# Kernel tuning notes

Measured on AMD Instinct MI355X. Metric: run time of the kernel, lower is better.

Reference implementation:

```python
import jax, jax.numpy as jnp
import numpy as np

H = 8          # num heads
D = 16         # head dim
HID = 128      # hidden_dim = H * D
NM, ND, NA = 100000, 20000, 50000
E = 300000     # edges per relation
NUM_CLASSES = 8


def setup_inputs() -> dict:
    key = jax.random.key(0)
    ks = jax.random.split(key, 24)
    s = 0.05
    eye = jnp.eye(D, dtype=jnp.float32)
    inp = {
        'x_movie': jax.random.normal(ks[0], (NM, 256), jnp.float32),
        'x_director': jax.random.normal(ks[1], (ND, 128), jnp.float32),
        'x_actor': jax.random.normal(ks[2], (NA, 128), jnp.float32),
        # edge lists per relation: (director->movie, actor->movie, movie->director, movie->actor)
        'src_dm': jax.random.randint(ks[3], (E,), 0, ND),
        'dst_dm': jax.random.randint(ks[4], (E,), 0, NM),
        'src_am': jax.random.randint(ks[5], (E,), 0, NA),
        'dst_am': jax.random.randint(ks[6], (E,), 0, NM),
        'src_md': jax.random.randint(ks[7], (E,), 0, NM),
        'dst_md': jax.random.randint(ks[8], (E,), 0, ND),
        'src_ma': jax.random.randint(ks[9], (E,), 0, NM),
        'dst_ma': jax.random.randint(ks[10], (E,), 0, NA),
        # per-type pre-encoder (use_pre_encoder=True)
        'Wpre_m': jax.random.normal(ks[11], (256, HID), jnp.float32) * s,
        'Wpre_d': jax.random.normal(ks[12], (128, HID), jnp.float32) * s,
        'Wpre_a': jax.random.normal(ks[13], (128, HID), jnp.float32) * s,
        'bpre': jnp.zeros((3, HID), jnp.float32),
        # per-type K/Q/V projections, stacked over the 3 node types
        'Wk': jax.random.normal(ks[14], (3, HID, HID), jnp.float32) * s,
        'bk': jnp.zeros((3, HID), jnp.float32),
        'Wq': jax.random.normal(ks[15], (3, HID, HID), jnp.float32) * s,
        'bq': jnp.zeros((3, HID), jnp.float32),
        'Wv': jax.random.normal(ks[16], (3, HID, HID), jnp.float32) * s,
        'bv': jnp.zeros((3, HID), jnp.float32),
        # per-relation attention / message matrices and priors (4 relations)
        'a_rel': eye + jax.random.normal(ks[17], (4, H, D, D), jnp.float32) * s,
        'm_rel': eye + jax.random.normal(ks[18], (4, H, D, D), jnp.float32) * s,
        'p_rel': jnp.ones((4, H), jnp.float32),
        # per-type skip gate and output projection
        'skip': jnp.ones((3,), jnp.float32),
        'Wa': jax.random.normal(ks[19], (3, HID, HID), jnp.float32) * s,
        'ba': jnp.zeros((3, HID), jnp.float32),
        # final classification head on target node type ('movie')
        'Wlin': jax.random.normal(ks[20], (HID, NUM_CLASSES), jnp.float32) * s,
        'blin': jnp.zeros((NUM_CLASSES,), jnp.float32),
    }
    return inp


def _seg_softmax_agg(alpha, msg, dst, n):
    # softmax over incoming edges of each destination node, then weighted sum of msgs
    m = jax.ops.segment_max(alpha, dst, num_segments=n)      # [n, H]
    m = jnp.where(jnp.isfinite(m), m, 0.0)
    a = jnp.exp(alpha - m[dst])                              # [E, H]
    denom = jax.ops.segment_sum(a, dst, num_segments=n)      # [n, H]
    num = jax.ops.segment_sum(a[:, :, None] * msg, dst, num_segments=n)  # [n, H, D]
    return num / jnp.maximum(denom, 1e-16)[:, :, None]


def reference(x_movie, x_director, x_actor,
              src_dm, dst_dm, src_am, dst_am, src_md, dst_md, src_ma, dst_ma,
              Wpre_m, Wpre_d, Wpre_a, bpre, Wk, bk, Wq, bq, Wv, bv,
              a_rel, m_rel, p_rel, skip, Wa, ba, Wlin, blin):
    # type order: 0=movie, 1=director, 2=actor
    xs = [x_movie @ Wpre_m + bpre[0],
          x_director @ Wpre_d + bpre[1],
          x_actor @ Wpre_a + bpre[2]]
    k = [(x @ Wk[t] + bk[t]).reshape(-1, H, D) for t, x in enumerate(xs)]
    q = [(x @ Wq[t] + bq[t]).reshape(-1, H, D) for t, x in enumerate(xs)]
    v = [(x @ Wv[t] + bv[t]).reshape(-1, H, D) for t, x in enumerate(xs)]

    # (src_type, dst_type, src_idx, dst_idx) per relation
    rels = [(1, 0, src_dm, dst_dm), (2, 0, src_am, dst_am),
            (0, 1, src_md, dst_md), (0, 2, src_ma, dst_ma)]
    scale = 1.0 / np.sqrt(D).astype(np.float32)
    buckets = {0: [], 1: [], 2: []}
    for r, (st, dt, src, dst) in enumerate(rels):
        ke = jnp.einsum('ehd,hdf->ehf', k[st][src], a_rel[r])          # [E,H,D]
        al = jnp.einsum('ehf,ehf->eh', q[dt][dst], ke) * p_rel[r] * scale
        me = jnp.einsum('ehd,hdf->ehf', v[st][src], m_rel[r])          # [E,H,D]
        buckets[dt].append((al, me, dst))

    n = [x.shape[0] for x in xs]
    outs = []
    for t in range(3):
        al = jnp.concatenate([b[0] for b in buckets[t]], axis=0)
        me = jnp.concatenate([b[1] for b in buckets[t]], axis=0)
        dst = jnp.concatenate([b[2] for b in buckets[t]], axis=0)
        agg = _seg_softmax_agg(al, me, dst, n[t]).reshape(n[t], HID)
        h = jax.nn.gelu(agg, approximate=False) @ Wa[t] + ba[t]
        g = jax.nn.sigmoid(skip[t])
        outs.append(g * h + (1.0 - g) * xs[t])

    return outs[0] @ Wlin + blin
```

## Files before the change

kernel.cpp:

```cpp
#include <hip/hip_runtime.h>
#include <hip/hip_bf16.h>
#include <math.h>

#define NM 100000
#define ND 20000
#define NA 50000
#define EDG 300000
#define CAP 32
#define NBLK_M 1563
#define NBLK_D 313
#define NBLK_A 782

typedef __attribute__((ext_vector_type(8))) short shortx8;
typedef __attribute__((ext_vector_type(4))) float floatx4;
typedef __attribute__((ext_vector_type(4))) int intx4;

__device__ __forceinline__ float bf2f(unsigned int u) {
    return __uint_as_float(u << 16);
}
__device__ __forceinline__ unsigned short f2bf(float f) {
    unsigned int x = __float_as_uint(f);
    unsigned int r = x + 0x7fffu + ((x >> 16) & 1u);
    return (unsigned short)(r >> 16);
}
__device__ __forceinline__ unsigned short f2bf_fast(float f) {
    return (unsigned short)((__float_as_uint(f) + 0x8000u) >> 16);
}
__device__ __forceinline__ unsigned int pkbf2(float a, float b) {
    return __builtin_amdgcn_perm(__float_as_uint(b) + 0x8000u,
                                 __float_as_uint(a) + 0x8000u,
                                 0x07060302u);
}
__device__ __forceinline__ float gelu_exact(float x) {
    return 0.5f * x * (1.0f + erff(x * 0.70710678118654752f));
}

static const size_t OFF_BT_Q      = 0;
static const size_t OFF_BT_KAMV_D = 73728;
static const size_t OFF_BT_KAMV_A = 139264;
static const size_t OFF_WKA_D     = 204800;
static const size_t OFF_WVM_D     = 270336;
static const size_t OFF_WKA_A     = 335872;
static const size_t OFF_WVM_A     = 401408;
static const size_t OFF_BQ        = 466944;
static const size_t OFF_B_KAMV_D  = 467520;
static const size_t OFF_B_KAMV_A  = 468544;
static const size_t OFF_BKA_D     = 469568;
static const size_t OFF_BVM_D     = 470080;
static const size_t OFF_BKA_A     = 470592;
static const size_t OFF_BVM_A     = 471104;
static const size_t OFF_WALS      = 471616;
static const size_t OFF_BFIN      = 475712;
static const size_t OFF_Q0        = 524288;
static const size_t OFF_SKIPB     = 26124288;
static const size_t OFF_WQT       = 26124288;
static const size_t OFF_KAMV_D    = 29324288;
static const size_t OFF_KAMV_A    = 39564288;
static const size_t OFF_COUNTS    = 65164288;
static const size_t OFF_SLOTS     = 65564288;
#define KAMV_A_DELTA 10240000

__global__ __launch_bounds__(256) void precompA(
    const float* __restrict__ Wk, const float* __restrict__ bk,
    const float* __restrict__ Wv, const float* __restrict__ bv,
    const float* __restrict__ Wa, const float* __restrict__ ba,
    const float* __restrict__ Wlin, const float* __restrict__ blin,
    const float* __restrict__ a_rel, const float* __restrict__ m_rel,
    const float* __restrict__ p_rel, const float* __restrict__ skip,
    const float* __restrict__ bpre, const float* __restrict__ Wq,
    char* __restrict__ ws)
{
    int tid = blockIdx.x * 256 + threadIdx.x;
    if (tid < 65536) {
        int mat = tid >> 14, rem = tid & 16383;
        int e = rem >> 7, hf = rem & 127, h = hf >> 4, f = hf & 15;
        const float* Wsrc; const float* R; float sc; float* dst;
        if (mat == 0)      { Wsrc = Wk + 16384; R = a_rel;        sc = p_rel[h]     * 0.25f; dst = (float*)(ws + OFF_WKA_D); }
        else if (mat == 1) { Wsrc = Wv + 16384; R = m_rel;        sc = 1.0f;                 dst = (float*)(ws + OFF_WVM_D); }
        else if (mat == 2) { Wsrc = Wk + 32768; R = a_rel + 2048; sc = p_rel[8 + h] * 0.25f; dst = (float*)(ws + OFF_WKA_A); }
        else               { Wsrc = Wv + 32768; R = m_rel + 2048; sc = 1.0f;                 dst = (float*)(ws + OFF_WVM_A); }
        float s = 0.0f;
        for (int d = 0; d < 16; d++)
            s += Wsrc[e * 128 + h * 16 + d] * R[h * 256 + d * 16 + f];
        dst[hf * 128 + e] = s * sc;
    } else if (tid < 66048) {
        int idx = tid - 65536;
        int mat = idx >> 7, hf = idx & 127, h = hf >> 4, f = hf & 15;
        const float* bsrc; const float* R; float sc; float* dst;
        if (mat == 0)      { bsrc = bk + 128; R = a_rel;        sc = p_rel[h]     * 0.25f; dst = (float*)(ws + OFF_BKA_D); }
        else if (mat == 1) { bsrc = bv + 128; R = m_rel;        sc = 1.0f;                 dst = (float*)(ws + OFF_BVM_D); }
        else if (mat == 2) { bsrc = bk + 256; R = a_rel + 2048; sc = p_rel[8 + h] * 0.25f; dst = (float*)(ws + OFF_BKA_A); }
        else               { bsrc = bv + 256; R = m_rel + 2048; sc = 1.0f;                 dst = (float*)(ws + OFF_BVM_A); }
        float s = 0.0f;
        for (int d = 0; d < 16; d++)
            s += bsrc[h * 16 + d] * R[h * 256 + d * 16 + f];
        dst[hf] = s * sc;
    } else if (tid < 67072) {
        int idx = tid - 66048;
        int j = idx >> 3, c = idx & 7;
        float g = 1.0f / (1.0f + __expf(-skip[0]));
        float s = 0.0f;
        for (int o = 0; o < 128; o++)
            s += Wa[j * 128 + o] * Wlin[o * 8 + c];
        ((float*)(ws + OFF_WALS))[j * 8 + c] = g * s;
    } else if (tid < 67080) {
        int c = tid - 67072;
        float g = 1.0f / (1.0f + __expf(-skip[0]));
        float s1 = 0.0f, s2 = 0.0f;
        for (int o = 0; o < 128; o++) {
            s1 += ba[o]   * Wlin[o * 8 + c];
            s2 += bpre[o] * Wlin[o * 8 + c];
        }
        ((float*)(ws + OFF_BFIN))[c] = g * s1 + (1.0f - g) * s2 + blin[c];
    } else if (tid < 83464) {
        int i = tid - 67080;
        int n = i >> 7, e = i & 127;
        ((float*)(ws + OFF_WQT))[n * 128 + e] = Wq[e * 128 + n];
    } else if (tid < 83464 + NM) {
        ((int*)(ws + OFF_COUNTS))[tid - 83464] = 0;
    }
}

__device__ __forceinline__ float dot128(const float* __restrict__ a,
                                        const float* __restrict__ b) {
    const floatx4* x = (const floatx4*)a;
    const floatx4* y = (const floatx4*)b;
    float s = 0.0f;
    #pragma unroll
    for (int i = 0; i < 32; i++) {
        floatx4 u = x[i], v = y[i];
        s += u[0] * v[0] + u[1] * v[1] + u[2] * v[2] + u[3] * v[3];
    }
    return s;
}

__global__ __launch_bounds__(256) void prep_scat(
    const int* __restrict__ src_dm, const int* __restrict__ dst_dm,
    const int* __restrict__ src_am, const int* __restrict__ dst_am,
    const float* __restrict__ Wpre_m, const float* __restrict__ Wpre_d,
    const float* __restrict__ Wpre_a, const float* __restrict__ bpre,
    const float* __restrict__ bq, const float* __restrict__ Wlin,
    const float* __restrict__ skip,
    char* __restrict__ ws)
{
    if (blockIdx.x < 2344) {
        int t = blockIdx.x * 256 + threadIdx.x;
        if (t >= 2 * EDG) return;
        int src, dst, delta;
        if (t < EDG) { src = src_dm[t];       dst = dst_dm[t];       delta = 0; }
        else         { src = src_am[t - EDG]; dst = dst_am[t - EDG]; delta = KAMV_A_DELTA; }
        int* counts = (int*)(ws + OFF_COUNTS);
        int* slots  = (int*)(ws + OFF_SLOTS);
        int pos = atomicAdd(&counts[dst], 1);
        if (pos < CAP) slots[(size_t)dst * CAP + pos] = src * 512 + delta;
        return;
    }
    int tid = (blockIdx.x - 2344) * 256 + threadIdx.x;
    const float* WKA_D = (const float*)(ws + OFF_WKA_D);
    const float* WVM_D = (const float*)(ws + OFF_WVM_D);
    const float* WKA_A = (const float*)(ws + OFF_WKA_A);
    const float* WVM_A = (const float*)(ws + OFF_WVM_A);
    const float* WqT   = (const float*)(ws + OFF_WQT);

    if (tid < 36864) {
        int n = tid >> 8, c = tid & 255;
        float s = 0.0f;
        if (n < 128) {
            s = dot128(Wpre_m + c * 128, WqT + n * 128);
        } else if (n < 136) {
            int cc = n - 128;
            float g = 1.0f / (1.0f + __expf(-skip[0]));
            for (int e = 0; e < 128; e++)
                s += Wpre_m[c * 128 + e] * Wlin[e * 8 + cc];
            s *= (1.0f - g);
        }
        ((unsigned short*)(ws + OFF_BT_Q))[(c >> 7) * 18432 + n * 128 + (c & 127)] = f2bf(s);
    } else if (tid < 69632) {
        int idx = tid - 36864;
        int nrow = idx >> 7, c = idx & 127;
        const float* WfT = (nrow < 128) ? WKA_D : WVM_D;
        int nc = nrow & 127;
        float s = dot128(Wpre_d + c * 128, WfT + nc * 128);
        ((unsigned short*)(ws + OFF_BT_KAMV_D))[nrow * 128 + c] = f2bf(s);
    } else if (tid < 102400) {
        int idx = tid - 69632;
        int nrow = idx >> 7, c = idx & 127;
        const float* WfT = (nrow < 128) ? WKA_A : WVM_A;
        int nc = nrow & 127;
        float s = dot128(Wpre_a + c * 128, WfT + nc * 128);
        ((unsigned short*)(ws + OFF_BT_KAMV_A))[nrow * 128 + c] = f2bf(s);
    } else if (tid < 102544) {
        int n = tid - 102400;
        float s = 0.0f;
        if (n < 128) s = dot128(bpre, WqT + n * 128) + bq[n];
        ((float*)(ws + OFF_BQ))[n] = s;
    } else if (tid < 102800) {
        int nrow = tid - 102544;
        const float* WfT = (nrow < 128) ? WKA_D : WVM_D;
        const float* bf_ = (nrow < 128) ? (const float*)(ws + OFF_BKA_D) : (const float*)(ws + OFF_BVM_D);
        int nc = nrow & 127;
        ((float*)(ws + OFF_B_KAMV_D))[nrow] = dot128(bpre + 128, WfT + nc * 128) + bf_[nc];
    } else if (tid < 103056) {
        int nrow = tid - 102800;
        const float* WfT = (nrow < 128) ? WKA_A : WVM_A;
        const float* bf_ = (nrow < 128) ? (const float*)(ws + OFF_BKA_A) : (const float*)(ws + OFF_BVM_A);
        int nc = nrow & 127;
        ((float*)(ws + OFF_B_KAMV_A))[nrow] = dot128(bpre + 256, WfT + nc * 128) + bf_[nc];
    }
}

#define MFMA16(a, b, c) __builtin_amdgcn_mfma_f32_16x16x32_bf16(a, b, c, 0, 0, 0)

__global__ __launch_bounds__(256, 2) void gemm_all(
    const float* __restrict__ xm, const float* __restrict__ xd,
    const float* __restrict__ xa,
    const unsigned short* __restrict__ btq,
    const unsigned short* __restrict__ btd,
    const unsigned short* __restrict__ bta,
    const float* __restrict__ bq,
    const float* __restrict__ bbd, const float* __restrict__ bba,
    unsigned short* __restrict__ q0, float* __restrict__ skipb,
    unsigned short* __restrict__ outd, unsigned short* __restrict__ outa)
{
    __shared__ unsigned short a_lds[64 * 136];
    __shared__ unsigned short b_lds[144 * 136];
    int tid = threadIdx.x;
    int w = tid >> 6, lane = tid & 63;
    int quad = lane >> 4, low = lane & 15;
    int bx = blockIdx.x;

    if (bx < NBLK_M) {
        int row0 = bx * 64;
        intx4 bv[9];
        #pragma unroll
        for (int it = 0; it < 9; it++) {
            int idx = it * 256 + tid, n = idx >> 4, ch = idx & 15;
            bv[it] = *(const intx4*)&btq[(size_t)n * 128 + ch * 8];
        }
        floatx4 av[8];
        #pragma unroll
        for (int it = 0; it < 8; it++) {
            int f = it * 256 + tid, r = f >> 5, c4 = f & 31;
            int rg = row0 + r; if (rg >= NM) rg = NM - 1;
            av[it] = *(const floatx4*)(xm + (size_t)rg * 256 + c4 * 4);
        }
        #pragma unroll
        for (int it = 0; it < 9; it++) {
            int idx = it * 256 + tid, n = idx >> 4, ch = idx & 15;
            *(intx4*)&b_lds[n * 136 + ch * 8] = bv[it];
        }
        #pragma unroll
        for (int it = 0; it < 8; it++) {
            int f = it * 256 + tid, r = f >> 5, c4 = f & 31;
            unsigned long long d =
                ((unsigned long long)pkbf2(av[it][2], av[it][3]) << 32) |
                pkbf2(av[it][0], av[it][1]);
            *(unsigned long long*)&a_lds[r * 136 + c4 * 4] = d;
        }
        __syncthreads();

        intx4 bv1[9];
        #pragma unroll
        for (int it = 0; it < 9; it++) {
            int idx = it * 256 + tid, n = idx >> 4, ch = idx & 15;
            bv1[it] = *(const intx4*)&btq[18432 + (size_t)n * 128 + ch * 8];
        }
        floatx4 av1[8];
        #pragma unroll
        for (int it = 0; it < 8; it++) {
            int f = it * 256 + tid, r = f >> 5, c4 = f & 31;
            int rg = row0 + r; if (rg >= NM) rg = NM - 1;
            av1[it] = *(const floatx4*)(xm + (size_t)rg * 256 + 128 + c4 * 4);
        }

        floatx4 acc[9] = {};
        #pragma unroll
        for (int ks = 0; ks < 4; ks++) {
            int ko = ks * 32 + quad * 8;
            shortx8 a0 = *(const shortx8*)&a_lds[(w * 16 + low) * 136 + ko];
            #pragma unroll
            for (int nt = 0; nt < 9; nt++) {
                shortx8 b = *(const shortx8*)&b_lds[(nt * 16 + low) * 136 + ko];
                acc[nt] = MFMA16(a0, b, acc[nt]);
            }
        }
        __syncthreads();
        #pragma unroll
        for (int it = 0; it < 9; it++) {
            int idx = it * 256 + tid, n = idx >> 4, ch = idx & 15;
            *(intx4*)&b_lds[n * 136 + ch * 8] = bv1[it];
        }
        #pragma unroll
        for (int it = 0; it < 8; it++) {
            int f = it * 256 + tid, r = f >> 5, c4 = f & 31;
            unsigned long long d =
                ((unsigned long long)pkbf2(av1[it][2], av1[it][3]) << 32) |
                pkbf2(av1[it][0], av1[it][1]);
            *(unsigned long long*)&a_lds[r * 136 + c4 * 4] = d;
        }
        __syncthreads();
        #pragma unroll
        for (int ks = 0; ks < 4; ks++) {
            int ko = ks * 32 + quad * 8;
            shortx8 a0 = *(const shortx8*)&a_lds[(w * 16 + low) * 136 + ko];
            #pragma unroll
            for (int nt = 0; nt < 9; nt++) {
                shortx8 b = *(const shortx8*)&b_lds[(nt * 16 + low) * 136 + ko];
                acc[nt] = MFMA16(a0, b, acc[nt]);
            }
        }

        int rb = row0 + w * 16;
        #pragma unroll
        for (int nt = 0; nt < 9; nt++) {
            #pragma unroll
            for (int r = 0; r < 4; r++) {
                int row = rb + quad * 4 + r;
                if (row >= NM) continue;
                int col = nt * 16 + low;
                float v = acc[nt][r] + bq[col];
                if (nt == 8) {
                    if (low < 8) skipb[(size_t)row * 8 + low] = v;
                } else {
                    q0[(size_t)row * 128 + col] = f2bf_fast(v);
                }
            }
        }
    } else {
        int rem = bx - NBLK_M;
        const float* A; const unsigned short* BT; const float* bias;
        unsigned short* outb; int M, kbx;
        if (rem < NBLK_D) { A = xd; BT = btd; bias = bbd; outb = outd; M = ND; kbx = rem; }
        else              { A = xa; BT = bta; bias = bba; outb = outa; M = NA; kbx = rem - NBLK_D; }
        int row0 = kbx * 64;

        intx4 bv[8];
        #pragma unroll
        for (int it = 0; it < 8; it++) {
            int idx = it * 256 + tid, n = idx >> 4, ch = idx & 15;
            bv[it] = *(const intx4*)&BT[(size_t)n * 128 + ch * 8];
        }
        floatx4 av[8];
        #pragma unroll
        for (int it = 0; it < 8; it++) {
            int f = it * 256 + tid, r = f >> 5, c4 = f & 31;
            int rg = row0 + r; if (rg >= M) rg = M - 1;
            av[it] = *(const floatx4*)(A + (size_t)rg * 128 + c4 * 4);
        }
        #pragma unroll
        for (int it = 0; it < 8; it++) {
            int idx = it * 256 + tid, n = idx >> 4, ch = idx & 15;
            *(intx4*)&b_lds[n * 136 + ch * 8] = bv[it];
        }
        #pragma unroll
        for (int it = 0; it < 8; it++) {
            int f = it * 256 + tid, r = f >> 5, c4 = f & 31;
            unsigned long long d =
                ((unsigned long long)pkbf2(av[it][2], av[it][3]) << 32) |
                pkbf2(av[it][0], av[it][1]);
            *(unsigned long long*)&a_lds[r * 136 + c4 * 4] = d;
        }
        __syncthreads();

        intx4 bv1[8];
        #pragma unroll
        for (int it = 0; it < 8; it++) {
            int idx = it * 256 + tid, n = idx >> 4, ch = idx & 15;
            bv1[it] = *(const intx4*)&BT[16384 + (size_t)n * 128 + ch * 8];
        }

        int rb = row0 + w * 16;
        {
            floatx4 acc[8] = {};
            #pragma unroll
            for (int ks = 0; ks < 4; ks++) {
                int ko = ks * 32 + quad * 8;
                shortx8 a0 = *(const shortx8*)&a_lds[(w * 16 + low) * 136 + ko];
                #pragma unroll
                for (int nt = 0; nt < 8; nt++) {
                    shortx8 b = *(const shortx8*)&b_lds[(nt * 16 + low) * 136 + ko];
                    acc[nt] = MFMA16(a0, b, acc[nt]);
                }
            }
            #pragma unroll
            for (int nt = 0; nt < 8; nt++) {
                #pragma unroll
                for (int r = 0; r < 4; r++) {
                    int row = rb + quad * 4 + r;
                    if (row >= M) continue;
                    int col = nt * 16 + low;
                    outb[(size_t)row * 256 + col] = f2bf_fast(acc[nt][r] + bias[col]);
                }
            }
        }
        __syncthreads();
        #pragma unroll
        for (int it = 0; it < 8; it++) {
            int idx = it * 256 + tid, n = idx >> 4, ch = idx & 15;
            *(intx4*)&b_lds[n * 136 + ch * 8] = bv1[it];
        }
        __syncthreads();
        {
            floatx4 acc[8] = {};
            #pragma unroll
            for (int ks = 0; ks < 4; ks++) {
                int ko = ks * 32 + quad * 8;
                shortx8 a0 = *(const shortx8*)&a_lds[(w * 16 + low) * 136 + ko];
                #pragma unroll
                for (int nt = 0; nt < 8; nt++) {
                    shortx8 b = *(const shortx8*)&b_lds[(nt * 16 + low) * 136 + ko];
                    acc[nt] = MFMA16(a0, b, acc[nt]);
                }
            }
            #pragma unroll
            for (int nt = 0; nt < 8; nt++) {
                #pragma unroll
                for (int r = 0; r < 4; r++) {
                    int row = rb + quad * 4 + r;
                    if (row >= M) continue;
                    int col = nt * 16 + low;
                    outb[(size_t)row * 256 + 128 + col] = f2bf_fast(acc[nt][r] + bias[128 + col]);
                }
            }
        }
    }
}

__global__ __launch_bounds__(256) void agg_kernel(
    const unsigned short* __restrict__ q0,
    const char* __restrict__ kamv0,
    const int* __restrict__ counts, const int* __restrict__ slots,
    const float* __restrict__ skipb,
    const float* __restrict__ WaLs, const float* __restrict__ bfin,
    float* __restrict__ out)
{
    __shared__ float wals[1032];
    for (int i = threadIdx.x; i < 1024; i += 256) {
        int c = i >> 7, rem = i & 127, j = rem >> 4, L = rem & 15;
        wals[i] = WaLs[(L * 8 + j) * 8 + c];
    }
    if (threadIdx.x < 8) wals[1024 + threadIdx.x] = bfin[threadIdx.x];
    __syncthreads();

    int lane = threadIdx.x & 63;
    int grp = lane >> 4;
    int L   = lane & 15;
    int n = blockIdx.x * 16 + (threadIdx.x >> 6) * 4 + grp;

    intx4 qv = *(const intx4*)(q0 + (size_t)n * 128 + L * 8);
    float qf[8];
    #pragma unroll
    for (int d = 0; d < 4; d++) {
        unsigned int u = (unsigned int)qv[d];
        qf[2 * d]     = __uint_as_float(u << 16);
        qf[2 * d + 1] = __uint_as_float(u & 0xffff0000u);
    }

    int cnt = counts[n];
    cnt = cnt < 0 ? 0 : (cnt > CAP ? CAP : cnt);
    int s0 = slots[(size_t)n * CAP + L];

    float acc[8] = {0, 0, 0, 0, 0, 0, 0, 0};
    float den = 0.0f;
    if (cnt > 0) {
        int off0 = __shfl(s0, lane & 48);
        const char* p = kamv0 + off0;
        intx4 ku = *(const intx4*)(p + L * 16);
        intx4 mu = *(const intx4*)(p + 256 + L * 16);
        for (int i = 0; i < cnt; i++) {
            int inext = (i + 1 < cnt) ? i + 1 : i;
            int offn = __shfl(s0, (lane & 48) + (inext & 15));
            if (__builtin_expect(inext >= 16, 0)) offn = slots[(size_t)n * CAP + inext];
            const char* pn = kamv0 + offn;
            intx4 kun = *(const intx4*)(pn + L * 16);
            intx4 mun = *(const intx4*)(pn + 256 + L * 16);

            float ph = 0.0f;
            #pragma unroll
            for (int d = 0; d < 4; d++) {
                unsigned int u = (unsigned int)ku[d];
                ph += qf[2 * d]     * __uint_as_float(u << 16);
                ph += qf[2 * d + 1] * __uint_as_float(u & 0xffff0000u);
            }
            float pf = ph + __shfl_xor(ph, 1);
            float wgt = __expf(fminf(pf, 60.0f));
            den += wgt;
            #pragma unroll
            for (int d = 0; d < 4; d++) {
                unsigned int u = (unsigned int)mu[d];
                acc[2 * d]     += wgt * __uint_as_float(u << 16);
                acc[2 * d + 1] += wgt * __uint_as_float(u & 0xffff0000u);
            }
            ku = kun; mu = mun;
        }
    }
    float inv = 1.0f / fmaxf(den, 1e-16f);

    float part[8] = {0, 0, 0, 0, 0, 0, 0, 0};
    #pragma unroll
    for (int j = 0; j < 8; j++) {
        float u = gelu_exact(acc[j] * inv);
        #pragma unroll
        for (int c = 0; c < 8; c++)
            part[c] += u * wals[c * 128 + j * 16 + L];
    }

    bool b0 = lane & 1, b1 = lane & 2, b2 = lane & 4;
    float t1[4], t2[2], t3;
    #pragma unroll
    for (int k = 0; k < 4; k++) {
        float send = b0 ? part[k] : part[4 + k];
        float got  = __shfl_xor(send, 1);
        t1[k] = (b0 ? part[4 + k] : part[k]) + got;
    }
    #pragma unroll
    for (int k = 0; k < 2; k++) {
        float send = b1 ? t1[k] : t1[2 + k];
        float got  = __shfl_xor(send, 2);
        t2[k] = (b1 ? t1[2 + k] : t1[k]) + got;
    }
    {
        float send = b2 ? t2[0] : t2[1];
        float got  = __shfl_xor(send, 4);
        t3 = (b2 ? t2[1] : t2[0]) + got;
    }
    t3 += __shfl_xor(t3, 8);
    if (L < 8) {
        int c = 4 * (L & 1) + 2 * ((L >> 1) & 1) + ((L >> 2) & 1);
        out[(size_t)n * 8 + c] = t3 + skipb[(size_t)n * 8 + c] + wals[1024 + c];
    }
}

extern "C" void kernel_launch(void* const* d_in, const int* in_sizes, int n_in,
                              void* d_out, int out_size, void* d_ws, size_t ws_size,
                              hipStream_t stream) {
    (void)in_sizes; (void)n_in; (void)out_size; (void)ws_size;
    const float* x_movie    = (const float*)d_in[0];
    const float* x_director = (const float*)d_in[1];
    const float* x_actor    = (const float*)d_in[2];
    const int* src_dm = (const int*)d_in[3];
    const int* dst_dm = (const int*)d_in[4];
    const int* src_am = (const int*)d_in[5];
    const int* dst_am = (const int*)d_in[6];
    const float* Wpre_m = (const float*)d_in[11];
    const float* Wpre_d = (const float*)d_in[12];
    const float* Wpre_a = (const float*)d_in[13];
    const float* bpre   = (const float*)d_in[14];
    const float* Wk     = (const float*)d_in[15];
    const float* bk     = (const float*)d_in[16];
    const float* Wq     = (const float*)d_in[17];
    const float* bq     = (const float*)d_in[18];
    const float* Wv     = (const float*)d_in[19];
    const float* bv     = (const float*)d_in[20];
    const float* a_rel  = (const float*)d_in[21];
    const float* m_rel  = (const float*)d_in[22];
    const float* p_rel  = (const float*)d_in[23];
    const float* skip   = (const float*)d_in[24];
    const float* Wa     = (const float*)d_in[25];
    const float* ba     = (const float*)d_in[26];
    const float* Wlin   = (const float*)d_in[27];
    const float* blin   = (const float*)d_in[28];

    char* ws = (char*)d_ws;
    float* out = (float*)d_out;

    precompA<<<(83464 + NM + 255) / 256, 256, 0, stream>>>(
        Wk, bk, Wv, bv, Wa, ba, Wlin, blin,
        a_rel, m_rel, p_rel, skip, bpre, Wq, ws);

    prep_scat<<<2344 + 403, 256, 0, stream>>>(
        src_dm, dst_dm, src_am, dst_am,
        Wpre_m, Wpre_d, Wpre_a, bpre, bq, Wlin, skip, ws);

    gemm_all<<<NBLK_M + NBLK_D + NBLK_A, 256, 0, stream>>>(
        x_movie, x_director, x_actor,
        (const unsigned short*)(ws + OFF_BT_Q),
        (const unsigned short*)(ws + OFF_BT_KAMV_D),
        (const unsigned short*)(ws + OFF_BT_KAMV_A),
        (const float*)(ws + OFF_BQ),
        (const float*)(ws + OFF_B_KAMV_D), (const float*)(ws + OFF_B_KAMV_A),
        (unsigned short*)(ws + OFF_Q0), (float*)(ws + OFF_SKIPB),
        (unsigned short*)(ws + OFF_KAMV_D), (unsigned short*)(ws + OFF_KAMV_A));

    agg_kernel<<<NM / 16, 256, 0, stream>>>(
        (const unsigned short*)(ws + OFF_Q0),
        (const char*)(ws + OFF_KAMV_D),
        (const int*)(ws + OFF_COUNTS), (const int*)(ws + OFF_SLOTS),
        (const float*)(ws + OFF_SKIPB),
        (const float*)(ws + OFF_WALS), (const float*)(ws + OFF_BFIN), out);
}
```

Before: 396.0 us.

## Make gemm_all persistent over 32-row tiles with register-prefetched next panel

Restructures the fused projection GEMM so each block loops over several 32-row tiles instead of one 64-row tile, and prefetches the next K-half or next tile's A and B data into registers while MFMAs run on the current LDS contents. Waves are split 2x2 over rows and column groups, the A tile is halved to raise occupancy to 3 blocks per CU, and the grid shrinks to about 760 blocks. The aim is to hide global load latency and cut the launch/tail cost of thousands of short blocks. In exchange, the B panel is reloaded from global memory for every tile and there are more barriers per output row, and the movie path drops the row bounds guard, relying on NM being divisible by 32.

```diff
diff --git a/kernel.cpp b/kernel.cpp
--- a/kernel.cpp
+++ b/kernel.cpp
@@ -7,9 +7,14 @@
 #define NA 50000
 #define EDG 300000
 #define CAP 32
-#define NBLK_M 1563
-#define NBLK_D 313
-#define NBLK_A 782
+
+#define NT_M   3125
+#define NT_D   625
+#define NT_K   2188
+#define T_M    7
+#define T_K    7
+#define BLK_M  447
+#define BLK_K  313
 
 typedef __attribute__((ext_vector_type(8))) short shortx8;
 typedef __attribute__((ext_vector_type(4))) float floatx4;
@@ -211,7 +216,7 @@
 
 #define MFMA16(a, b, c) __builtin_amdgcn_mfma_f32_16x16x32_bf16(a, b, c, 0, 0, 0)
 
-__global__ __launch_bounds__(256, 2) void gemm_all(
+__global__ __launch_bounds__(256, 3) void gemm_all(
     const float* __restrict__ xm, const float* __restrict__ xd,
     const float* __restrict__ xa,
     const unsigned short* __restrict__ btq,
@@ -222,204 +227,194 @@
     unsigned short* __restrict__ q0, float* __restrict__ skipb,
     unsigned short* __restrict__ outd, unsigned short* __restrict__ outa)
 {
-    __shared__ unsigned short a_lds[64 * 136];
+    __shared__ unsigned short a_lds[32 * 136];
     __shared__ unsigned short b_lds[144 * 136];
     int tid = threadIdx.x;
     int w = tid >> 6, lane = tid & 63;
     int quad = lane >> 4, low = lane & 15;
+    int g = w >> 1, s = w & 1;
     int bx = blockIdx.x;
 
-    if (bx < NBLK_M) {
-        int row0 = bx * 64;
+    if (bx < BLK_M) {
+        int tbase = bx * T_M;
+        floatx4 av[4];
         intx4 bv[9];
-        #pragma unroll
-        for (int it = 0; it < 9; it++) {
-            int idx = it * 256 + tid, n = idx >> 4, ch = idx & 15;
-            bv[it] = *(const intx4*)&btq[(size_t)n * 128 + ch * 8];
-        }
-        floatx4 av[8];
-        #pragma unroll
-        for (int it = 0; it < 8; it++) {
-            int f = it * 256 + tid, r = f >> 5, c4 = f & 31;
-            int rg = row0 + r; if (rg >= NM) rg = NM - 1;
-            av[it] = *(const floatx4*)(xm + (size_t)rg * 256 + c4 * 4);
-        }
-        #pragma unroll
-        for (int it = 0; it < 9; it++) {
-            int idx = it * 256 + tid, n = idx >> 4, ch = idx & 15;
-            *(intx4*)&b_lds[n * 136 + ch * 8] = bv[it];
-        }
-        #pragma unroll
-        for (int it = 0; it < 8; it++) {
-            int f = it * 256 + tid, r = f >> 5, c4 = f & 31;
-            unsigned long long d =
-                ((unsigned long long)pkbf2(av[it][2], av[it][3]) << 32) |
-                pkbf2(av[it][0], av[it][1]);
-            *(unsigned long long*)&a_lds[r * 136 + c4 * 4] = d;
-        }
-        __syncthreads();
-
-        intx4 bv1[9];
-        #pragma unroll
-        for (int it = 0; it < 9; it++) {
-            int idx = it * 256 + tid, n = idx >> 4, ch = idx & 15;
-            bv1[it] = *(const intx4*)&btq[18432 + (size_t)n * 128 + ch * 8];
-        }
-        floatx4 av1[8];
-        #pragma unroll
-        for (int it = 0; it < 8; it++) {
-            int f = it * 256 + tid, r = f >> 5, c4 = f & 31;
-            int rg = row0 + r; if (rg >= NM) rg = NM - 1;
-            av1[it] = *(const floatx4*)(xm + (size_t)rg * 256 + 128 + c4 * 4);
-        }
-
-        floatx4 acc[9] = {};
-        #pragma unroll
-        for (int ks = 0; ks < 4; ks++) {
-            int ko = ks * 32 + quad * 8;
-            shortx8 a0 = *(const shortx8*)&a_lds[(w * 16 + low) * 136 + ko];
-            #pragma unroll
-            for (int nt = 0; nt < 9; nt++) {
-                shortx8 b = *(const shortx8*)&b_lds[(nt * 16 + low) * 136 + ko];
-                acc[nt] = MFMA16(a0, b, acc[nt]);
-            }
-        }
-        __syncthreads();
-        #pragma unroll
-        for (int it = 0; it < 9; it++) {
-            int idx = it * 256 + tid, n = idx >> 4, ch = idx & 15;
-            *(intx4*)&b_lds[n * 136 + ch * 8] = bv1[it];
-        }
-        #pragma unroll
-        for (int it = 0; it < 8; it++) {
-            int f = it * 256 + tid, r = f >> 5, c4 = f & 31;
-            unsigned long long d =
-                ((unsigned long long)pkbf2(av1[it][2], av1[it][3]) << 32) |
-                pkbf2(av1[it][0], av1[it][1]);
-            *(unsigned long long*)&a_lds[r * 136 + c4 * 4] = d;
-        }
-        __syncthreads();
-        #pragma unroll
-        for (int ks = 0; ks < 4; ks++) {
-            int ko = ks * 32 + quad * 8;
-            shortx8 a0 = *(const shortx8*)&a_lds[(w * 16 + low) * 136 + ko];
-            #pragma unroll
-            for (int nt = 0; nt < 9; nt++) {
-                shortx8 b = *(const shortx8*)&b_lds[(nt * 16 + low) * 136 + ko];
-                acc[nt] = MFMA16(a0, b, acc[nt]);
-            }
-        }
-
-        int rb = row0 + w * 16;
-        #pragma unroll
-        for (int nt = 0; nt < 9; nt++) {
-            #pragma unroll
-            for (int r = 0; r < 4; r++) {
-                int row = rb + quad * 4 + r;
-                if (row >= NM) continue;
+        {
+            int row0 = (tbase < NT_M ? tbase : NT_M - 1) * 32;
+            #pragma unroll
+            for (int it = 0; it < 4; it++) {
+                int f = it * 256 + tid, r = f >> 5, c4 = f & 31;
+                av[it] = *(const floatx4*)(xm + (size_t)(row0 + r) * 256 + c4 * 4);
+            }
+            #pragma unroll
+            for (int it = 0; it < 9; it++) {
+                int idx = it * 256 + tid, n = idx >> 4, ch = idx & 15;
+                bv[it] = *(const intx4*)&btq[(size_t)n * 128 + ch * 8];
+            }
+        }
+        for (int t = 0; t < T_M; t++) {
+            int tcur = tbase + t;
+            if (tcur >= NT_M) break;
+            int row0 = tcur * 32;
+            floatx4 acc[5] = {};
+            #pragma unroll
+            for (int h = 0; h < 2; h++) {
+                __syncthreads();
+                #pragma unroll
+                for (int it = 0; it < 4; it++) {
+                    int f = it * 256 + tid, r = f >> 5, c4 = f & 31;
+                    unsigned long long d =
+                        ((unsigned long long)pkbf2(av[it][2], av[it][3]) << 32) |
+                        pkbf2(av[it][0], av[it][1]);
+                    *(unsigned long long*)&a_lds[r * 136 + c4 * 4] = d;
+                }
+                #pragma unroll
+                for (int it = 0; it < 9; it++) {
+                    int idx = it * 256 + tid, n = idx >> 4, ch = idx & 15;
+                    *(intx4*)&b_lds[n * 136 + ch * 8] = bv[it];
+                }
+                __syncthreads();
+                {
+                    int ntile = (h == 0) ? tcur : (tcur + 1 < NT_M ? tcur + 1 : NT_M - 1);
+                    int nh = 1 - h;
+                    int nrow0 = ntile * 32;
+                    #pragma unroll
+                    for (int it = 0; it < 4; it++) {
+                        int f = it * 256 + tid, r = f >> 5, c4 = f & 31;
+                        av[it] = *(const floatx4*)(xm + (size_t)(nrow0 + r) * 256 + nh * 128 + c4 * 4);
+                    }
+                    #pragma unroll
+                    for (int it = 0; it < 9; it++) {
+                        int idx = it * 256 + tid, n = idx >> 4, ch = idx & 15;
+                        bv[it] = *(const intx4*)&btq[(size_t)nh * 18432 + n * 128 + ch * 8];
+                    }
+                }
+                #pragma unroll
+                for (int ks = 0; ks < 4; ks++) {
+                    int ko = ks * 32 + quad * 8;
+                    shortx8 a0 = *(const shortx8*)&a_lds[(s * 16 + low) * 136 + ko];
+                    #pragma unroll
+                    for (int j = 0; j < 5; j++) {
+                        if (g == 1 && j == 4) continue;
+                        int nt = g * 5 + j;
+                        shortx8 b = *(const shortx8*)&b_lds[(nt * 16 + low) * 136 + ko];
+                        acc[j] = MFMA16(a0, b, acc[j]);
+                    }
+                }
+            }
+            #pragma unroll
+            for (int j = 0; j < 5; j++) {
+                if (g == 1 && j == 4) continue;
+                int nt = g * 5 + j;
                 int col = nt * 16 + low;
-                float v = acc[nt][r] + bq[col];
-                if (nt == 8) {
-                    if (low < 8) skipb[(size_t)row * 8 + low] = v;
+                #pragma unroll
+                for (int r = 0; r < 4; r++) {
+                    int row = row0 + s * 16 + quad * 4 + r;
+                    float v = acc[j][r] + bq[col];
+                    if (nt == 8) {
+                        if (low < 8) skipb[(size_t)row * 8 + low] = v;
+                    } else {
+                        q0[(size_t)row * 128 + col] = f2bf_fast(v);
+                    }
+                }
+            }
+        }
+    } else {
+        int kbase = (bx - BLK_M) * T_K;
+        floatx4 av[4];
+        intx4 bv[8];
+        {
+            int tt = kbase < NT_K ? kbase : NT_K - 1;
+            const float* A; int M, row0;
+            const unsigned short* BT;
+            if (tt < NT_D) { A = xd; M = ND; row0 = tt * 32; BT = btd; }
+            else           { A = xa; M = NA; row0 = (tt - NT_D) * 32; BT = bta; }
+            #pragma unroll
+            for (int it = 0; it < 4; it++) {
+                int f = it * 256 + tid, r = f >> 5, c4 = f & 31;
+                int rg = row0 + r; if (rg >= M) rg = M - 1;
+                av[it] = *(const floatx4*)(A + (size_t)rg * 128 + c4 * 4);
+            }
+            #pragma unroll
+            for (int it = 0; it < 8; it++) {
+                int idx = it * 256 + tid, n = idx >> 4, ch = idx & 15;
+                bv[it] = *(const intx4*)&BT[(size_t)n * 128 + ch * 8];
+            }
+        }
+        for (int t = 0; t < T_K; t++) {
+            int tcur = kbase + t;
+            if (tcur >= NT_K) break;
+            const float* A; int M, row0;
+            const unsigned short* BT; const float* bias;
+            unsigned short* outb;
+            if (tcur < NT_D) { A = xd; M = ND; row0 = tcur * 32; BT = btd; bias = bbd; outb = outd; }
+            else             { A = xa; M = NA; row0 = (tcur - NT_D) * 32; BT = bta; bias = bba; outb = outa; }
+
+            #pragma unroll
+            for (int pnl = 0; pnl < 2; pnl++) {
+                __syncthreads();
+                if (pnl == 0) {
+                    #pragma unroll
+                    for (int it = 0; it < 4; it++) {
+                        int f = it * 256 + tid, r = f >> 5, c4 = f & 31;
+                        unsigned long long d =
+                            ((unsigned long long)pkbf2(av[it][2], av[it][3]) << 32) |
+                            pkbf2(av[it][0], av[it][1]);
+                        *(unsigned long long*)&a_lds[r * 136 + c4 * 4] = d;
+                    }
+                }
+                #pragma unroll
+                for (int it = 0; it < 8; it++) {
+                    int idx = it * 256 + tid, n = idx >> 4, ch = idx & 15;
+                    *(intx4*)&b_lds[n * 136 + ch * 8] = bv[it];
+                }
+                __syncthreads();
+                if (pnl == 0) {
+                    #pragma unroll
+                    for (int it = 0; it < 8; it++) {
+                        int idx = it * 256 + tid, n = idx >> 4, ch = idx & 15;
+                        bv[it] = *(const intx4*)&BT[16384 + (size_t)n * 128 + ch * 8];
+                    }
                 } else {
-                    q0[(size_t)row * 128 + col] = f2bf_fast(v);
-                }
-            }
-        }
-    } else {
-        int rem = bx - NBLK_M;
-        const float* A; const unsigned short* BT; const float* bias;
-        unsigned short* outb; int M, kbx;
-        if (rem < NBLK_D) { A = xd; BT = btd; bias = bbd; outb = outd; M = ND; kbx = rem; }
-        else              { A = xa; BT = bta; bias = bba; outb = outa; M = NA; kbx = rem - NBLK_D; }
-        int row0 = kbx * 64;
-
-        intx4 bv[8];
-        #pragma unroll
-        for (int it = 0; it < 8; it++) {
-            int idx = it * 256 + tid, n = idx >> 4, ch = idx & 15;
-            bv[it] = *(const intx4*)&BT[(size_t)n * 128 + ch * 8];
-        }
-        floatx4 av[8];
-        #pragma unroll
-        for (int it = 0; it < 8; it++) {
-            int f = it * 256 + tid, r = f >> 5, c4 = f & 31;
-            int rg = row0 + r; if (rg >= M) rg = M - 1;
-            av[it] = *(const floatx4*)(A + (size_t)rg * 128 + c4 * 4);
-        }
-        #pragma unroll
-        for (int it = 0; it < 8; it++) {
-            int idx = it * 256 + tid, n = idx >> 4, ch = idx & 15;
-            *(intx4*)&b_lds[n * 136 + ch * 8] = bv[it];
-        }
-        #pragma unroll
-        for (int it = 0; it < 8; it++) {
-            int f = it * 256 + tid, r = f >> 5, c4 = f & 31;
-            unsigned long long d =
-                ((unsigned long long)pkbf2(av[it][2], av[it][3]) << 32) |
-                pkbf2(av[it][0], av[it][1]);
-            *(unsigned long long*)&a_lds[r * 136 + c4 * 4] = d;
-        }
-        __syncthreads();
-
-        intx4 bv1[8];
-        #pragma unroll
-        for (int it = 0; it < 8; it++) {
-            int idx = it * 256 + tid, n = idx >> 4, ch = idx & 15;
-            bv1[it] = *(const intx4*)&BT[16384 + (size_t)n * 128 + ch * 8];
-        }
-
-        int rb = row0 + w * 16;
-        {
-            floatx4 acc[8] = {};
-            #pragma unroll
-            for (int ks = 0; ks < 4; ks++) {
-                int ko = ks * 32 + quad * 8;
-                shortx8 a0 = *(const shortx8*)&a_lds[(w * 16 + low) * 136 + ko];
-                #pragma unroll
-                for (int nt = 0; nt < 8; nt++) {
-                    shortx8 b = *(const shortx8*)&b_lds[(nt * 16 + low) * 136 + ko];
-                    acc[nt] = MFMA16(a0, b, acc[nt]);
-                }
-            }
-            #pragma unroll
-            for (int nt = 0; nt < 8; nt++) {
-                #pragma unroll
-                for (int r = 0; r < 4; r++) {
-                    int row = rb + quad * 4 + r;
-                    if (row >= M) continue;
-                    int col = nt * 16 + low;
-                    outb[(size_t)row * 256 + col] = f2bf_fast(acc[nt][r] + bias[col]);
-                }
-            }
-        }
-        __syncthreads();
-        #pragma unroll
-        for (int it = 0; it < 8; it++) {
-            int idx = it * 256 + tid, n = idx >> 4, ch = idx & 15;
-            *(intx4*)&b_lds[n * 136 + ch * 8] = bv1[it];
-        }
-        __syncthreads();
-        {
-            floatx4 acc[8] = {};
-            #pragma unroll
-            for (int ks = 0; ks < 4; ks++) {
-                int ko = ks * 32 + quad * 8;
-                shortx8 a0 = *(const shortx8*)&a_lds[(w * 16 + low) * 136 + ko];
-                #pragma unroll
-                for (int nt = 0; nt < 8; nt++) {
-                    shortx8 b = *(const shortx8*)&b_lds[(nt * 16 + low) * 136 + ko];
-                    acc[nt] = MFMA16(a0, b, acc[nt]);
-                }
-            }
-            #pragma unroll
-            for (int nt = 0; nt < 8; nt++) {
-                #pragma unroll
-                for (int r = 0; r < 4; r++) {
-                    int row = rb + quad * 4 + r;
-                    if (row >= M) continue;
-                    int col = nt * 16 + low;
-                    outb[(size_t)row * 256 + 128 + col] = f2bf_fast(acc[nt][r] + bias[128 + col]);
+                    int tn = (tcur + 1 < NT_K) ? tcur + 1 : NT_K - 1;
+                    const float* An; int Mn, nrow0;
+                    const unsigned short* BTn;
+                    if (tn < NT_D) { An = xd; Mn = ND; nrow0 = tn * 32; BTn = btd; }
+                    else           { An = xa; Mn = NA; nrow0 = (tn - NT_D) * 32; BTn = bta; }
+                    #pragma unroll
+                    for (int it = 0; it < 4; it++) {
+                        int f = it * 256 + tid, r = f >> 5, c4 = f & 31;
+                        int rg = nrow0 + r; if (rg >= Mn) rg = Mn - 1;
+                        av[it] = *(const floatx4*)(An + (size_t)rg * 128 + c4 * 4);
+                    }
+                    #pragma unroll
+                    for (int it = 0; it < 8; it++) {
+                        int idx = it * 256 + tid, n = idx >> 4, ch = idx & 15;
+                        bv[it] = *(const intx4*)&BTn[(size_t)n * 128 + ch * 8];
+                    }
+                }
+                floatx4 acc[4] = {};
+                #pragma unroll
+                for (int ks = 0; ks < 4; ks++) {
+                    int ko = ks * 32 + quad * 8;
+                    shortx8 a0 = *(const shortx8*)&a_lds[(s * 16 + low) * 136 + ko];
+                    #pragma unroll
+                    for (int j = 0; j < 4; j++) {
+                        int nt = g * 4 + j;
+                        shortx8 b = *(const shortx8*)&b_lds[(nt * 16 + low) * 136 + ko];
+                        acc[j] = MFMA16(a0, b, acc[j]);
+                    }
+                }
+                #pragma unroll
+                for (int j = 0; j < 4; j++) {
+                    int nt = g * 4 + j;
+                    int col = pnl * 128 + nt * 16 + low;
+                    #pragma unroll
+                    for (int r = 0; r < 4; r++) {
+                        int row = row0 + s * 16 + quad * 4 + r;
+                        if (row < M)
+                            outb[(size_t)row * 256 + col] = f2bf_fast(acc[j][r] + bias[pnl * 128 + nt * 16 + low]);
+                    }
                 }
             }
         }
@@ -572,7 +567,7 @@
         src_dm, dst_dm, src_am, dst_am,
         Wpre_m, Wpre_d, Wpre_a, bpre, bq, Wlin, skip, ws);
 
-    gemm_all<<<NBLK_M + NBLK_D + NBLK_A, 256, 0, stream>>>(
+    gemm_all<<<BLK_M + BLK_K, 256, 0, stream>>>(
         x_movie, x_director, x_actor,
         (const unsigned short*)(ws + OFF_BT_Q),
         (const unsigned short*)(ws + OFF_BT_KAMV_D),
```

After: 394.4 us. Within noise of the previous version (-0.4%).
